# Optimization experiments

Measured on AMD Instinct MI355X. Metric: run time of the kernel, lower is better.

The kernel has to match this reference:

```python
import jax, jax.numpy as jnp
import numpy as np

B, S, D = 2, 2048, 1024
H, L = 16, 64  # num_heads, latent_dim (head dim); head_dim = H*L = 1024
ROPE_BASE = 10000.0


def _rope_tables(seq_len, dim):
    inv_freq = 1.0 / (ROPE_BASE ** (2.0 * jnp.arange(0, dim // 2, dtype=jnp.float32) / dim))
    pos = jnp.arange(seq_len, dtype=jnp.float32)
    ang = pos[:, None] * inv_freq[None, :]           # [S, L/2]
    cos = jnp.cos(ang).reshape(1, seq_len, 1, dim // 2)
    sin = jnp.sin(ang).reshape(1, seq_len, 1, dim // 2)
    return cos, sin


def _apply_rope(t, cos, sin):
    # t: [B, S, H, L]; interleaved-pair rotation then concat halves (as in source)
    tr = t.reshape(*t.shape[:-1], -1, 2)             # [B,S,H,L/2,2]
    x0, x1 = tr[..., 0], tr[..., 1]
    out = jnp.concatenate([x0 * cos - x1 * sin, x0 * sin + x1 * cos], axis=-1)
    return out.reshape(t.shape)


def setup_inputs() -> dict:
    key = jax.random.key(0)
    ks = jax.random.split(key, 5)
    scale = 0.03  # ~xavier for 1024x1024
    return {
        "x": jax.random.normal(ks[0], (B, S, D), dtype=jnp.float32),
        "Wq": jax.random.normal(ks[1], (D, H * L), dtype=jnp.float32) * scale,
        "bq": jnp.zeros((H * L,), dtype=jnp.float32),
        "Wk": jax.random.normal(ks[2], (D, H * L), dtype=jnp.float32) * scale,
        "bk": jnp.zeros((H * L,), dtype=jnp.float32),
        "Wv": jax.random.normal(ks[3], (D, H * L), dtype=jnp.float32) * scale,
        "bv": jnp.zeros((H * L,), dtype=jnp.float32),
        "Wo": jax.random.normal(ks[4], (H * L, D), dtype=jnp.float32) * scale,
        "bo": jnp.zeros((D,), dtype=jnp.float32),
    }


def reference(x, Wq, bq, Wk, bk, Wv, bv, Wo, bo):
    b, s, _ = x.shape
    q = (x @ Wq + bq).reshape(b, s, H, L)
    k = (x @ Wk + bk).reshape(b, s, H, L)
    v = (x @ Wv + bv).reshape(b, s, H, L)
    cos, sin = _rope_tables(s, L)
    q = _apply_rope(q, cos, sin)
    k = _apply_rope(k, cos, sin)
    q = jnp.transpose(q, (0, 2, 1, 3))  # [B,H,S,L]
    k = jnp.transpose(k, (0, 2, 1, 3))
    v = jnp.transpose(v, (0, 2, 1, 3))
    scores = jnp.einsum('bnqd,bnkd->bnqk', q, k) / jnp.sqrt(jnp.float32(L))
    # causal mask: keep positions where key <= query
    causal = jnp.arange(s)[None, :] <= jnp.arange(s)[:, None]  # [S,S]
    scores = jnp.where(causal, scores, -1e9)
    attn = jax.nn.softmax(scores, axis=-1)
    attended = jnp.einsum('bnqk,bnkd->bnqd', attn, v)
    attended = jnp.transpose(attended, (0, 2, 1, 3)).reshape(b, s, H * L)
    return attended @ Wo + bo
```

## Files before the change

### kernel.cpp

```cpp
#include <hip/hip_runtime.h>
#include <hip/hip_bf16.h>

typedef __bf16 bf16_t;
typedef __bf16 bf16x2 __attribute__((ext_vector_type(2)));
typedef __bf16 bf16x4 __attribute__((ext_vector_type(4)));
typedef __bf16 bf16x8 __attribute__((ext_vector_type(8)));
typedef float  f32x4  __attribute__((ext_vector_type(4)));

#define GLDS16(gp, lp) __builtin_amdgcn_global_load_lds( \
    (const __attribute__((address_space(1))) void*)(gp), \
    (__attribute__((address_space(3))) void*)(lp), 16, 0, 0)

#define MFMA16(a, b, c) __builtin_amdgcn_mfma_f32_16x16x32_bf16((a), (b), (c), 0, 0, 0)

static constexpr int kB = 2, kS = 2048, kD = 1024, kH = 16, kL = 64;
static constexpr int kM = kB * kS;
static constexpr int kNqkv = 3 * kD;
static constexpr int kBH = kB * kH;

__global__ void cast_x_kernel(const float* __restrict__ x, bf16_t* __restrict__ xb) {
    int i = blockIdx.x * 256 + threadIdx.x;
    float4 v = ((const float4*)x)[i];
    bf16x4 o;
    o[0] = (bf16_t)v.x; o[1] = (bf16_t)v.y; o[2] = (bf16_t)v.z; o[3] = (bf16_t)v.w;
    ((bf16x4*)xb)[i] = o;
}

__global__ void wtrans_kernel(const float* __restrict__ W, bf16_t* __restrict__ Wt) {
    __shared__ float t[32 * 33];
    const int k0 = blockIdx.x * 32, n0 = blockIdx.y * 32;
    const int tid = threadIdx.x;
#pragma unroll
    for (int i = 0; i < 4; ++i) {
        int idx = i * 256 + tid;
        int r = idx >> 5, c = idx & 31;
        t[r * 33 + c] = W[(size_t)(k0 + r) * 1024 + n0 + c];
    }
    __syncthreads();
#pragma unroll
    for (int i = 0; i < 4; ++i) {
        int idx = i * 256 + tid;
        int r = idx >> 5, c = idx & 31;
        Wt[(size_t)(n0 + r) * 1024 + k0 + c] = (bf16_t)t[c * 33 + r];
    }
}

__global__ void rope_table_kernel(float* __restrict__ cosT, float* __restrict__ sinT) {
    int i = blockIdx.x * 256 + threadIdx.x;
    int s = i >> 5, j = i & 31;
    double inv = pow(10000.0, -2.0 * (double)j / 64.0);
    double ang = (double)s * inv;
    cosT[i] = (float)cos(ang);
    sinT[i] = (float)sin(ang);
}

template <int MODE>
__global__ __launch_bounds__(256, 2)
void gemm_bf16(const bf16_t* __restrict__ A, const bf16_t* __restrict__ Bt,
               void* __restrict__ Cout,
               const float* __restrict__ b0, const float* __restrict__ b1,
               const float* __restrict__ b2, int Ndim, int Kdim) {
    __shared__ __align__(16) bf16_t Alds[128 * 32];
    __shared__ __align__(16) bf16_t Blds[128 * 32];
    const int tid = threadIdx.x;
    const int lane = tid & 63;
    const int wid = tid >> 6;
    const int lo = lane & 15, hi = lane >> 4;
    const int bm = blockIdx.x, bn = blockIdx.y;
    const int wr = wid >> 1, wc = wid & 1;

    const int rowS = (wid * 2) * 16 + (lane >> 2);
    const int colE = (lane & 3) * 8;
    const bf16_t* gA0 = A + (size_t)(bm * 128 + rowS) * Kdim + colE;
    const bf16_t* gA1 = gA0 + (size_t)16 * Kdim;
    const bf16_t* gB0 = Bt + (size_t)(bn * 128 + rowS) * Kdim + colE;
    const bf16_t* gB1 = gB0 + (size_t)16 * Kdim;
    bf16_t* lA0 = &Alds[(wid * 2) * 512];
    bf16_t* lA1 = &Alds[(wid * 2 + 1) * 512];
    bf16_t* lB0 = &Blds[(wid * 2) * 512];
    bf16_t* lB1 = &Blds[(wid * 2 + 1) * 512];

    f32x4 acc[4][4];
#pragma unroll
    for (int m = 0; m < 4; ++m)
#pragma unroll
        for (int n = 0; n < 4; ++n) acc[m][n] = (f32x4){0.f, 0.f, 0.f, 0.f};

    const int nk = Kdim >> 5;
    for (int kt = 0; kt < nk; ++kt) {
        const int k0 = kt * 32;
        GLDS16(gA0 + k0, lA0);
        GLDS16(gA1 + k0, lA1);
        GLDS16(gB0 + k0, lB0);
        GLDS16(gB1 + k0, lB1);
        __syncthreads();
        bf16x8 aF[4], bF[4];
#pragma unroll
        for (int m = 0; m < 4; ++m)
            aF[m] = *(const bf16x8*)&Alds[(wr * 64 + m * 16 + lo) * 32 + hi * 8];
#pragma unroll
        for (int n = 0; n < 4; ++n)
            bF[n] = *(const bf16x8*)&Blds[(wc * 64 + n * 16 + lo) * 32 + hi * 8];
#pragma unroll
        for (int m = 0; m < 4; ++m)
#pragma unroll
            for (int n = 0; n < 4; ++n)
                acc[m][n] = MFMA16(aF[m], bF[n], acc[m][n]);
        __syncthreads();
    }

    const int rbase = bm * 128 + wr * 64 + hi * 4;
    const int cbase = bn * 128 + wc * 64 + lo;
    if (MODE == 0) {
        bf16_t* C = (bf16_t*)Cout;
#pragma unroll
        for (int m = 0; m < 4; ++m)
#pragma unroll
            for (int n = 0; n < 4; ++n) {
                const int col = cbase + n * 16;
                const float bias = (col < 1024) ? b0[col]
                                 : (col < 2048) ? b1[col - 1024] : b2[col - 2048];
#pragma unroll
                for (int r = 0; r < 4; ++r) {
                    const int row = rbase + m * 16 + r;
                    C[(size_t)row * Ndim + col] = (bf16_t)(acc[m][n][r] + bias);
                }
            }
    } else {
        float* C = (float*)Cout;
#pragma unroll
        for (int m = 0; m < 4; ++m)
#pragma unroll
            for (int n = 0; n < 4; ++n) {
                const int col = cbase + n * 16;
                const float bias = b0[col];
#pragma unroll
                for (int r = 0; r < 4; ++r) {
                    const int row = rbase + m * 16 + r;
                    C[(size_t)row * Ndim + col] = acc[m][n][r] + bias;
                }
            }
    }
}

__global__ __launch_bounds__(256)
void rope_qk_kernel(const bf16_t* __restrict__ qkv,
                    const float* __restrict__ cosT,
                    const float* __restrict__ sinT,
                    bf16_t* __restrict__ Qr, bf16_t* __restrict__ Kr) {
    const int st = blockIdx.x, bh = blockIdx.y;
    const int b = bh >> 4, h = bh & 15;
    const int tid = threadIdx.x;
    const int r = tid >> 2;
    const int part = tid & 3;
    const int s = st * 64 + r;
    const int bs = b * kS + s;
    const bf16_t* qp = qkv + (size_t)bs * kNqkv + h * 64 + part * 16;
    const bf16_t* kp = qp + 1024;
    const size_t outoff = ((size_t)(b * kH + h) * kS + s) * 64;
    bf16_t* qo = Qr + outoff;
    char*   kob = (char*)(Kr + outoff);
    const float* cr = cosT + s * 32 + part * 8;
    const float* sr = sinT + s * 32 + part * 8;
    const float kScale = 0.125f * 1.44269504f;

    bf16x8 q0 = *(const bf16x8*)qp;
    bf16x8 q1 = *(const bf16x8*)(qp + 8);
    bf16x8 k0 = *(const bf16x8*)kp;
    bf16x8 k1 = *(const bf16x8*)(kp + 8);
    bf16x8 qlo, qhi, klo, khi;
#pragma unroll
    for (int j = 0; j < 8; ++j) {
        const float cv = cr[j];
        const float sv = sr[j];
        float qa, qb2, ka, kb2;
        if (j < 4) {
            qa = (float)q0[2 * j];     qb2 = (float)q0[2 * j + 1];
            ka = (float)k0[2 * j];     kb2 = (float)k0[2 * j + 1];
        } else {
            qa = (float)q1[2 * j - 8]; qb2 = (float)q1[2 * j - 7];
            ka = (float)k1[2 * j - 8]; kb2 = (float)k1[2 * j - 7];
        }
        qlo[j] = (bf16_t)((qa * cv - qb2 * sv) * kScale);
        qhi[j] = (bf16_t)((qa * sv + qb2 * cv) * kScale);
        klo[j] = (bf16_t)(ka * cv - kb2 * sv);
        khi[j] = (bf16_t)(ka * sv + kb2 * cv);
    }
    *(bf16x8*)(qo + part * 8)      = qlo;
    *(bf16x8*)(qo + 32 + part * 8) = qhi;
    const int sw = s & 7;
    *(bf16x8*)(kob + (((part)     ^ sw) << 4)) = klo;
    *(bf16x8*)(kob + (((part + 4) ^ sw) << 4)) = khi;
}

__global__ void vtrans_kernel(const bf16_t* __restrict__ qkv, bf16_t* __restrict__ VT) {
    __shared__ __align__(16) bf16_t t[64 * 72];
    const int st = blockIdx.x, bh = blockIdx.y;
    const int b = bh >> 4, h = bh & 15;
    const int tid = threadIdx.x;
    const int r = tid >> 2, g = tid & 3;
    const bf16_t* src = qkv + ((size_t)(b * kS + st * 64 + r)) * kNqkv + 2048 + h * 64 + g * 16;
    bf16x8 v0 = *(const bf16x8*)src;
    bf16x8 v1 = *(const bf16x8*)(src + 8);
    *(bf16x8*)&t[r * 72 + g * 16] = v0;
    *(bf16x8*)&t[r * 72 + g * 16 + 8] = v1;
    __syncthreads();
    bf16x8 o0, o1;
#pragma unroll
    for (int j = 0; j < 8; ++j) {
        o0[j] = t[(g * 16 + j) * 72 + r];
        o1[j] = t[(g * 16 + 8 + j) * 72 + r];
    }
    char* dstb = (char*)(VT + ((size_t)bh * 64 + r) * kS) + st * 128;
    const int sw = r & 7;
    *(bf16x8*)(dstb + (((g * 2)     ^ sw) << 4)) = o0;
    *(bf16x8*)(dstb + (((g * 2 + 1) ^ sw) << 4)) = o1;
}

__global__ __launch_bounds__(256, 2)
void attn_kernel(const bf16_t* __restrict__ Qr, const bf16_t* __restrict__ Kr,
                 const bf16_t* __restrict__ VT, bf16_t* __restrict__ attended) {
    __shared__ __align__(16) bf16_t Klds[2][64 * 64];
    __shared__ __align__(16) bf16_t Vlds[2][64 * 64];
    __shared__ __align__(16) bf16_t Plds[8][16 * 72];
    const int qp = blockIdx.x, bh = blockIdx.y;
    const int qA = qp, qB = 31 - qp;
    const int tid = threadIdx.x;
    const int lane = tid & 63, wid = tid >> 6;
    const int lo = lane & 15, hi = lane >> 4;
    const int q0A = qA * 64 + wid * 16;
    const int q0B = qB * 64 + wid * 16;

    const char* Kg = (const char*)(Kr + (size_t)bh * kS * 64);
    const char* Vg = (const char*)(VT + (size_t)bh * 64 * kS);
    const bf16_t* Q = Qr + (size_t)bh * kS * 64;

    const bf16x8 aQA0 = *(const bf16x8*)&Q[(size_t)(q0A + lo) * 64 + hi * 8];
    const bf16x8 aQA1 = *(const bf16x8*)&Q[(size_t)(q0A + lo) * 64 + 32 + hi * 8];
    const bf16x8 aQB0 = *(const bf16x8*)&Q[(size_t)(q0B + lo) * 64 + hi * 8];
    const bf16x8 aQB1 = *(const bf16x8*)&Q[(size_t)(q0B + lo) * 64 + 32 + hi * 8];

    f32x4 OA[4], OB[4];
#pragma unroll
    for (int dt = 0; dt < 4; ++dt) {
        OA[dt] = (f32x4){0.f, 0.f, 0.f, 0.f};
        OB[dt] = (f32x4){0.f, 0.f, 0.f, 0.f};
    }
    float mA = -1e30f, lA = 0.f, mB = -1e30f, lB = 0.f;

    auto stage = [&](int buf, int t) {
        char* Kl = (char*)&Klds[buf][0];
        char* Vl = (char*)&Vlds[buf][0];
        const size_t kb = (size_t)t * 128 * 64;
        const int vcol = t * 128;
#pragma unroll
        for (int j = 0; j < 2; ++j) {
            const int seg = wid * 2 + j;
            GLDS16(Kg + kb + seg * 1024 + lane * 16, Kl + seg * 1024);
            const int row = seg * 8 + (lane >> 3);
            GLDS16(Vg + (size_t)row * (kS * 2) + vcol + (lane & 7) * 16, Vl + seg * 1024);
        }
    };

    auto softmax = [&](f32x4 (&s)[4], float& m_run, float& l_run, f32x4 (&O)[4],
                       int q0, bool edge, int kv0, bf16_t* Pl,
                       bf16x8& aP0, bf16x8& aP1) {
        if (edge) {
            const int qg = q0 + lo;
#pragma unroll
            for (int ct = 0; ct < 4; ++ct)
#pragma unroll
                for (int r = 0; r < 4; ++r)
                    if (kv0 + ct * 16 + hi * 4 + r > qg) s[ct][r] = -1e30f;
        }
        float pmax = -1e30f;
#pragma unroll
        for (int ct = 0; ct < 4; ++ct)
#pragma unroll
            for (int r = 0; r < 4; ++r) pmax = fmaxf(pmax, s[ct][r]);
        pmax = fmaxf(pmax, __shfl_xor(pmax, 16, 64));
        pmax = fmaxf(pmax, __shfl_xor(pmax, 32, 64));
        if (!__all(pmax - m_run <= 8.0f)) {
            const float mn = fmaxf(m_run, pmax);
            const float alpha = exp2f(m_run - mn);
            m_run = mn;
            l_run *= alpha;
            float av[4];
#pragma unroll
            for (int r = 0; r < 4; ++r) av[r] = __shfl(alpha, hi * 4 + r, 64);
#pragma unroll
            for (int dt = 0; dt < 4; ++dt)
#pragma unroll
                for (int r = 0; r < 4; ++r) O[dt][r] *= av[r];
        }
        float psum = 0.f;
#pragma unroll
        for (int ct = 0; ct < 4; ++ct)
#pragma unroll
            for (int r = 0; r < 4; ++r) {
                const float e = exp2f(s[ct][r] - m_run);
                s[ct][r] = e;
                psum += e;
            }
        psum += __shfl_xor(psum, 16, 64);
        psum += __shfl_xor(psum, 32, 64);
        l_run += psum;
#pragma unroll
        for (int ct = 0; ct < 4; ++ct)
#pragma unroll
            for (int rp = 0; rp < 2; ++rp) {
                bf16x2 v;
                v[0] = (bf16_t)s[ct][2 * rp];
                v[1] = (bf16_t)s[ct][2 * rp + 1];
                *(bf16x2*)&Pl[lo * 72 + ct * 16 + hi * 4 + 2 * rp] = v;
            }
        aP0 = *(const bf16x8*)&Pl[lo * 72 + hi * 8];
        aP1 = *(const bf16x8*)&Pl[lo * 72 + 32 + hi * 8];
    };

    stage(0, 0);
    int cur = 0;
    for (int t = 0; t <= qB; ++t) {
        __syncthreads();
        if (t < qB) stage(cur ^ 1, t + 1);
        const char* Kb = (const char*)&Klds[cur][0];
        const char* Vb = (const char*)&Vlds[cur][0];
        const bool actA = (t <= qA);
        const int kv0 = t * 64;

        f32x4 sB[4], sA[4];
#pragma unroll
        for (int ct = 0; ct < 4; ++ct) {
            sB[ct] = (f32x4){0.f, 0.f, 0.f, 0.f};
            sA[ct] = (f32x4){0.f, 0.f, 0.f, 0.f};
        }
#pragma unroll
        for (int ct = 0; ct < 4; ++ct) {
            const int rr = ct * 16 + lo;
            const bf16x8 bK0 = *(const bf16x8*)(Kb + rr * 128 + (((hi)     ^ (rr & 7)) << 4));
            const bf16x8 bK1 = *(const bf16x8*)(Kb + rr * 128 + (((hi + 4) ^ (rr & 7)) << 4));
            sB[ct] = MFMA16(bK0, aQB0, sB[ct]);
            sB[ct] = MFMA16(bK1, aQB1, sB[ct]);
            if (actA) {
                sA[ct] = MFMA16(bK0, aQA0, sA[ct]);
                sA[ct] = MFMA16(bK1, aQA1, sA[ct]);
            }
        }

        bf16x8 aP0A, aP1A, aP0B, aP1B;
        if (actA) softmax(sA, mA, lA, OA, q0A, t == qA, kv0, &Plds[wid * 2][0], aP0A, aP1A);
        softmax(sB, mB, lB, OB, q0B, t == qB, kv0, &Plds[wid * 2 + 1][0], aP0B, aP1B);

#pragma unroll
        for (int dt = 0; dt < 4; ++dt) {
            const int rr = dt * 16 + lo;
            const bf16x8 bV0 = *(const bf16x8*)(Vb + rr * 128 + (((hi)     ^ (rr & 7)) << 4));
            const bf16x8 bV1 = *(const bf16x8*)(Vb + rr * 128 + (((hi + 4) ^ (rr & 7)) << 4));
            OB[dt] = MFMA16(aP0B, bV0, OB[dt]);
            OB[dt] = MFMA16(aP1B, bV1, OB[dt]);
            if (actA) {
                OA[dt] = MFMA16(aP0A, bV0, OA[dt]);
                OA[dt] = MFMA16(aP1A, bV1, OA[dt]);
            }
        }
        cur ^= 1;
    }

    const int b = bh >> 4, h = bh & 15;
    float liA[4], liB[4];
#pragma unroll
    for (int r = 0; r < 4; ++r) {
        liA[r] = 1.0f / __shfl(lA, hi * 4 + r, 64);
        liB[r] = 1.0f / __shfl(lB, hi * 4 + r, 64);
    }
#pragma unroll
    for (int dt = 0; dt < 4; ++dt)
#pragma unroll
        for (int r = 0; r < 4; ++r) {
            const int rowA = q0A + hi * 4 + r;
            const int rowB = q0B + hi * 4 + r;
            attended[((size_t)(b * kS + rowA)) * kD + h * 64 + dt * 16 + lo] =
                (bf16_t)(OA[dt][r] * liA[r]);
            attended[((size_t)(b * kS + rowB)) * kD + h * 64 + dt * 16 + lo] =
                (bf16_t)(OB[dt][r] * liB[r]);
        }
}

extern "C" void kernel_launch(void* const* d_in, const int* in_sizes, int n_in,
                              void* d_out, int out_size, void* d_ws, size_t ws_size,
                              hipStream_t stream) {
    const float* x  = (const float*)d_in[0];
    const float* Wq = (const float*)d_in[1];
    const float* bq = (const float*)d_in[2];
    const float* Wk = (const float*)d_in[3];
    const float* bk = (const float*)d_in[4];
    const float* Wv = (const float*)d_in[5];
    const float* bv = (const float*)d_in[6];
    const float* Wo = (const float*)d_in[7];
    const float* bo = (const float*)d_in[8];
    float* out = (float*)d_out;

    char* ws = (char*)d_ws;
    size_t off = 0;
    auto carve = [&](size_t bytes) -> char* {
        char* p = ws + off;
        off += (bytes + 255) & ~(size_t)255;
        return p;
    };
    bf16_t* xb    = (bf16_t*)carve((size_t)kM * kD * 2);
    bf16_t* WqkvT = (bf16_t*)carve((size_t)kNqkv * kD * 2);
    bf16_t* WoT   = (bf16_t*)carve((size_t)kD * kD * 2);
    float*  cosT  = (float*)carve((size_t)kS * 32 * 4);
    float*  sinT  = (float*)carve((size_t)kS * 32 * 4);
    bf16_t* qkv   = (bf16_t*)carve((size_t)kM * kNqkv * 2);
    bf16_t* Qr    = (bf16_t*)carve((size_t)kBH * kS * 64 * 2);
    bf16_t* Kr    = (bf16_t*)carve((size_t)kBH * kS * 64 * 2);
    bf16_t* VT    = (bf16_t*)carve((size_t)kBH * kS * 64 * 2);
    bf16_t* att   = (bf16_t*)carve((size_t)kM * kD * 2);

    cast_x_kernel<<<(kM * kD) / (256 * 4), 256, 0, stream>>>(x, xb);
    wtrans_kernel<<<dim3(32, 32), 256, 0, stream>>>(Wq, WqkvT);
    wtrans_kernel<<<dim3(32, 32), 256, 0, stream>>>(Wk, WqkvT + (size_t)1024 * 1024);
    wtrans_kernel<<<dim3(32, 32), 256, 0, stream>>>(Wv, WqkvT + (size_t)2048 * 1024);
    wtrans_kernel<<<dim3(32, 32), 256, 0, stream>>>(Wo, WoT);
    rope_table_kernel<<<(kS * 32) / 256, 256, 0, stream>>>(cosT, sinT);

    gemm_bf16<0><<<dim3(kM / 128, kNqkv / 128), 256, 0, stream>>>(
        xb, WqkvT, qkv, bq, bk, bv, kNqkv, kD);

    rope_qk_kernel<<<dim3(kS / 64, kBH), 256, 0, stream>>>(qkv, cosT, sinT, Qr, Kr);
    vtrans_kernel<<<dim3(kS / 64, kBH), 256, 0, stream>>>(qkv, VT);

    attn_kernel<<<dim3(16, kBH), 256, 0, stream>>>(Qr, Kr, VT, att);

    gemm_bf16<1><<<dim3(kM / 128, kD / 128), 256, 0, stream>>>(
        att, WoT, out, bo, nullptr, nullptr, kD, kD);
}
```

Measured before the change: 147.1 us.

## Load K and V fragments directly from global memory instead of LDS staging

Removes the double-buffered LDS staging of K and V tiles in the attention kernel. Each wave now loads its MFMA operand fragments straight from global memory into registers, and the XOR swizzle is dropped from the rope and V-transpose writers to match. It also raises wave priority around the MFMA sections with s_setprio. This drops block-wide barriers and LDS traffic, but each wave of the block now fetches the same K/V data, so it depends on L1/L2 hits and exposes global load latency without a prefetch.

```diff
diff --git a/kernel.cpp b/kernel.cpp
--- a/kernel.cpp
+++ b/kernel.cpp
@@ -159,7 +159,7 @@
     const bf16_t* kp = qp + 1024;
     const size_t outoff = ((size_t)(b * kH + h) * kS + s) * 64;
     bf16_t* qo = Qr + outoff;
-    char*   kob = (char*)(Kr + outoff);
+    bf16_t* ko = Kr + outoff;
     const float* cr = cosT + s * 32 + part * 8;
     const float* sr = sinT + s * 32 + part * 8;
     const float kScale = 0.125f * 1.44269504f;
@@ -188,9 +188,8 @@
     }
     *(bf16x8*)(qo + part * 8)      = qlo;
     *(bf16x8*)(qo + 32 + part * 8) = qhi;
-    const int sw = s & 7;
-    *(bf16x8*)(kob + (((part)     ^ sw) << 4)) = klo;
-    *(bf16x8*)(kob + (((part + 4) ^ sw) << 4)) = khi;
+    *(bf16x8*)(ko + part * 8)      = klo;
+    *(bf16x8*)(ko + 32 + part * 8) = khi;
 }
 
 __global__ void vtrans_kernel(const bf16_t* __restrict__ qkv, bf16_t* __restrict__ VT) {
@@ -211,17 +210,14 @@
         o0[j] = t[(g * 16 + j) * 72 + r];
         o1[j] = t[(g * 16 + 8 + j) * 72 + r];
     }
-    char* dstb = (char*)(VT + ((size_t)bh * 64 + r) * kS) + st * 128;
-    const int sw = r & 7;
-    *(bf16x8*)(dstb + (((g * 2)     ^ sw) << 4)) = o0;
-    *(bf16x8*)(dstb + (((g * 2 + 1) ^ sw) << 4)) = o1;
+    bf16_t* dst = VT + ((size_t)bh * 64 + r) * kS + st * 64 + g * 16;
+    *(bf16x8*)dst = o0;
+    *(bf16x8*)(dst + 8) = o1;
 }
 
 __global__ __launch_bounds__(256, 2)
 void attn_kernel(const bf16_t* __restrict__ Qr, const bf16_t* __restrict__ Kr,
                  const bf16_t* __restrict__ VT, bf16_t* __restrict__ attended) {
-    __shared__ __align__(16) bf16_t Klds[2][64 * 64];
-    __shared__ __align__(16) bf16_t Vlds[2][64 * 64];
     __shared__ __align__(16) bf16_t Plds[8][16 * 72];
     const int qp = blockIdx.x, bh = blockIdx.y;
     const int qA = qp, qB = 31 - qp;
@@ -231,9 +227,9 @@
     const int q0A = qA * 64 + wid * 16;
     const int q0B = qB * 64 + wid * 16;
 
-    const char* Kg = (const char*)(Kr + (size_t)bh * kS * 64);
-    const char* Vg = (const char*)(VT + (size_t)bh * 64 * kS);
-    const bf16_t* Q = Qr + (size_t)bh * kS * 64;
+    const bf16_t* Kp = Kr + (size_t)bh * kS * 64;
+    const bf16_t* Vp = VT + (size_t)bh * 64 * kS;
+    const bf16_t* Q  = Qr + (size_t)bh * kS * 64;
 
     const bf16x8 aQA0 = *(const bf16x8*)&Q[(size_t)(q0A + lo) * 64 + hi * 8];
     const bf16x8 aQA1 = *(const bf16x8*)&Q[(size_t)(q0A + lo) * 64 + 32 + hi * 8];
@@ -247,20 +243,6 @@
         OB[dt] = (f32x4){0.f, 0.f, 0.f, 0.f};
     }
     float mA = -1e30f, lA = 0.f, mB = -1e30f, lB = 0.f;
-
-    auto stage = [&](int buf, int t) {
-        char* Kl = (char*)&Klds[buf][0];
-        char* Vl = (char*)&Vlds[buf][0];
-        const size_t kb = (size_t)t * 128 * 64;
-        const int vcol = t * 128;
-#pragma unroll
-        for (int j = 0; j < 2; ++j) {
-            const int seg = wid * 2 + j;
-            GLDS16(Kg + kb + seg * 1024 + lane * 16, Kl + seg * 1024);
-            const int row = seg * 8 + (lane >> 3);
-            GLDS16(Vg + (size_t)row * (kS * 2) + vcol + (lane & 7) * 16, Vl + seg * 1024);
-        }
-    };
 
     auto softmax = [&](f32x4 (&s)[4], float& m_run, float& l_run, f32x4 (&O)[4],
                        int q0, bool edge, int kv0, bf16_t* Pl,
@@ -318,15 +300,17 @@
         aP1 = *(const bf16x8*)&Pl[lo * 72 + 32 + hi * 8];
     };
 
-    stage(0, 0);
-    int cur = 0;
     for (int t = 0; t <= qB; ++t) {
-        __syncthreads();
-        if (t < qB) stage(cur ^ 1, t + 1);
-        const char* Kb = (const char*)&Klds[cur][0];
-        const char* Vb = (const char*)&Vlds[cur][0];
+        const int kv0 = t * 64;
         const bool actA = (t <= qA);
-        const int kv0 = t * 64;
+
+        bf16x8 bK0[4], bK1[4];
+#pragma unroll
+        for (int ct = 0; ct < 4; ++ct) {
+            const bf16_t* kr = Kp + (size_t)(kv0 + ct * 16 + lo) * 64 + hi * 8;
+            bK0[ct] = *(const bf16x8*)kr;
+            bK1[ct] = *(const bf16x8*)(kr + 32);
+        }
 
         f32x4 sB[4], sA[4];
 #pragma unroll
@@ -334,36 +318,41 @@
             sB[ct] = (f32x4){0.f, 0.f, 0.f, 0.f};
             sA[ct] = (f32x4){0.f, 0.f, 0.f, 0.f};
         }
+        __builtin_amdgcn_s_setprio(1);
 #pragma unroll
         for (int ct = 0; ct < 4; ++ct) {
-            const int rr = ct * 16 + lo;
-            const bf16x8 bK0 = *(const bf16x8*)(Kb + rr * 128 + (((hi)     ^ (rr & 7)) << 4));
-            const bf16x8 bK1 = *(const bf16x8*)(Kb + rr * 128 + (((hi + 4) ^ (rr & 7)) << 4));
-            sB[ct] = MFMA16(bK0, aQB0, sB[ct]);
-            sB[ct] = MFMA16(bK1, aQB1, sB[ct]);
+            sB[ct] = MFMA16(bK0[ct], aQB0, sB[ct]);
+            sB[ct] = MFMA16(bK1[ct], aQB1, sB[ct]);
             if (actA) {
-                sA[ct] = MFMA16(bK0, aQA0, sA[ct]);
-                sA[ct] = MFMA16(bK1, aQA1, sA[ct]);
-            }
+                sA[ct] = MFMA16(bK0[ct], aQA0, sA[ct]);
+                sA[ct] = MFMA16(bK1[ct], aQA1, sA[ct]);
+            }
+        }
+        __builtin_amdgcn_s_setprio(0);
+
+        bf16x8 bV0[4], bV1[4];
+#pragma unroll
+        for (int dt = 0; dt < 4; ++dt) {
+            const bf16_t* vr = Vp + (size_t)(dt * 16 + lo) * kS + kv0 + hi * 8;
+            bV0[dt] = *(const bf16x8*)vr;
+            bV1[dt] = *(const bf16x8*)(vr + 32);
         }
 
         bf16x8 aP0A, aP1A, aP0B, aP1B;
         if (actA) softmax(sA, mA, lA, OA, q0A, t == qA, kv0, &Plds[wid * 2][0], aP0A, aP1A);
         softmax(sB, mB, lB, OB, q0B, t == qB, kv0, &Plds[wid * 2 + 1][0], aP0B, aP1B);
 
+        __builtin_amdgcn_s_setprio(1);
 #pragma unroll
         for (int dt = 0; dt < 4; ++dt) {
-            const int rr = dt * 16 + lo;
-            const bf16x8 bV0 = *(const bf16x8*)(Vb + rr * 128 + (((hi)     ^ (rr & 7)) << 4));
-            const bf16x8 bV1 = *(const bf16x8*)(Vb + rr * 128 + (((hi + 4) ^ (rr & 7)) << 4));
-            OB[dt] = MFMA16(aP0B, bV0, OB[dt]);
-            OB[dt] = MFMA16(aP1B, bV1, OB[dt]);
+            OB[dt] = MFMA16(aP0B, bV0[dt], OB[dt]);
+            OB[dt] = MFMA16(aP1B, bV1[dt], OB[dt]);
             if (actA) {
-                OA[dt] = MFMA16(aP0A, bV0, OA[dt]);
-                OA[dt] = MFMA16(aP1A, bV1, OA[dt]);
-            }
-        }
-        cur ^= 1;
+                OA[dt] = MFMA16(aP0A, bV0[dt], OA[dt]);
+                OA[dt] = MFMA16(aP1A, bV1[dt], OA[dt]);
+            }
+        }
+        __builtin_amdgcn_s_setprio(0);
     }
 
     const int b = bh >> 4, h = bh & 15;
```

Measured after the change: 205.8 us. 1.4x slower.

## Replace paired-tile attention blocks with one query tile per block, heavy-first order

Applied to the files above, without the earlier changes.

The attention kernel stops pairing query tiles qp and 31-qp in each block and gives each block a single 64-row query tile. The grid becomes (32 heads*batch, 32 tiles), with the longest causal tiles dispatched first, and launch bounds are raised to allow 4 blocks per CU. MFMA sections are wrapped in s_setprio hints, and the P scratch buffer loses its padding. This doubles the block count and cuts per-block registers to improve occupancy and load balance. In exchange, K/V tiles are no longer shared between two query tiles, so global and LDS traffic increases, and the unpadded P layout may cause bank conflicts.

```diff
diff --git a/kernel.cpp b/kernel.cpp
--- a/kernel.cpp
+++ b/kernel.cpp
@@ -217,36 +217,32 @@
     *(bf16x8*)(dstb + (((g * 2 + 1) ^ sw) << 4)) = o1;
 }
 
-__global__ __launch_bounds__(256, 2)
+__global__ __launch_bounds__(256, 4)
 void attn_kernel(const bf16_t* __restrict__ Qr, const bf16_t* __restrict__ Kr,
                  const bf16_t* __restrict__ VT, bf16_t* __restrict__ attended) {
     __shared__ __align__(16) bf16_t Klds[2][64 * 64];
     __shared__ __align__(16) bf16_t Vlds[2][64 * 64];
-    __shared__ __align__(16) bf16_t Plds[8][16 * 72];
-    const int qp = blockIdx.x, bh = blockIdx.y;
-    const int qA = qp, qB = 31 - qp;
+    __shared__ __align__(16) bf16_t Plds[4][16 * 64];
+    const int bh = blockIdx.x;
+    const int qt = 31 - blockIdx.y;
     const int tid = threadIdx.x;
     const int lane = tid & 63, wid = tid >> 6;
     const int lo = lane & 15, hi = lane >> 4;
-    const int q0A = qA * 64 + wid * 16;
-    const int q0B = qB * 64 + wid * 16;
+    const int q0 = qt * 64 + wid * 16;
 
     const char* Kg = (const char*)(Kr + (size_t)bh * kS * 64);
     const char* Vg = (const char*)(VT + (size_t)bh * 64 * kS);
     const bf16_t* Q = Qr + (size_t)bh * kS * 64;
 
-    const bf16x8 aQA0 = *(const bf16x8*)&Q[(size_t)(q0A + lo) * 64 + hi * 8];
-    const bf16x8 aQA1 = *(const bf16x8*)&Q[(size_t)(q0A + lo) * 64 + 32 + hi * 8];
-    const bf16x8 aQB0 = *(const bf16x8*)&Q[(size_t)(q0B + lo) * 64 + hi * 8];
-    const bf16x8 aQB1 = *(const bf16x8*)&Q[(size_t)(q0B + lo) * 64 + 32 + hi * 8];
-
-    f32x4 OA[4], OB[4];
-#pragma unroll
-    for (int dt = 0; dt < 4; ++dt) {
-        OA[dt] = (f32x4){0.f, 0.f, 0.f, 0.f};
-        OB[dt] = (f32x4){0.f, 0.f, 0.f, 0.f};
-    }
-    float mA = -1e30f, lA = 0.f, mB = -1e30f, lB = 0.f;
+    const bf16x8 aQ0 = *(const bf16x8*)&Q[(size_t)(q0 + lo) * 64 + hi * 8];
+    const bf16x8 aQ1 = *(const bf16x8*)&Q[(size_t)(q0 + lo) * 64 + 32 + hi * 8];
+
+    bf16_t* Pl = &Plds[wid][0];
+
+    f32x4 O[4];
+#pragma unroll
+    for (int dt = 0; dt < 4; ++dt) O[dt] = (f32x4){0.f, 0.f, 0.f, 0.f};
+    float m_run = -1e30f, l_run = 0.f;
 
     auto stage = [&](int buf, int t) {
         char* Kl = (char*)&Klds[buf][0];
@@ -262,9 +258,31 @@
         }
     };
 
-    auto softmax = [&](f32x4 (&s)[4], float& m_run, float& l_run, f32x4 (&O)[4],
-                       int q0, bool edge, int kv0, bf16_t* Pl,
-                       bf16x8& aP0, bf16x8& aP1) {
+    stage(0, 0);
+    int cur = 0;
+    const int ntiles = qt + 1;
+    for (int t = 0; t < ntiles; ++t) {
+        __syncthreads();
+        if (t + 1 < ntiles) stage(cur ^ 1, t + 1);
+        const char* Kb = (const char*)&Klds[cur][0];
+        const char* Vb = (const char*)&Vlds[cur][0];
+        const int kv0 = t * 64;
+        const bool edge = (t == qt);
+
+        f32x4 s[4];
+#pragma unroll
+        for (int ct = 0; ct < 4; ++ct) s[ct] = (f32x4){0.f, 0.f, 0.f, 0.f};
+        __builtin_amdgcn_s_setprio(1);
+#pragma unroll
+        for (int ct = 0; ct < 4; ++ct) {
+            const int rr = ct * 16 + lo;
+            const bf16x8 bK0 = *(const bf16x8*)(Kb + rr * 128 + (((hi)     ^ (rr & 7)) << 4));
+            const bf16x8 bK1 = *(const bf16x8*)(Kb + rr * 128 + (((hi + 4) ^ (rr & 7)) << 4));
+            s[ct] = MFMA16(bK0, aQ0, s[ct]);
+            s[ct] = MFMA16(bK1, aQ1, s[ct]);
+        }
+        __builtin_amdgcn_s_setprio(0);
+
         if (edge) {
             const int qg = q0 + lo;
 #pragma unroll
@@ -312,77 +330,35 @@
                 bf16x2 v;
                 v[0] = (bf16_t)s[ct][2 * rp];
                 v[1] = (bf16_t)s[ct][2 * rp + 1];
-                *(bf16x2*)&Pl[lo * 72 + ct * 16 + hi * 4 + 2 * rp] = v;
+                *(bf16x2*)&Pl[lo * 64 + ct * 16 + hi * 4 + 2 * rp] = v;
             }
-        aP0 = *(const bf16x8*)&Pl[lo * 72 + hi * 8];
-        aP1 = *(const bf16x8*)&Pl[lo * 72 + 32 + hi * 8];
-    };
-
-    stage(0, 0);
-    int cur = 0;
-    for (int t = 0; t <= qB; ++t) {
-        __syncthreads();
-        if (t < qB) stage(cur ^ 1, t + 1);
-        const char* Kb = (const char*)&Klds[cur][0];
-        const char* Vb = (const char*)&Vlds[cur][0];
-        const bool actA = (t <= qA);
-        const int kv0 = t * 64;
-
-        f32x4 sB[4], sA[4];
-#pragma unroll
-        for (int ct = 0; ct < 4; ++ct) {
-            sB[ct] = (f32x4){0.f, 0.f, 0.f, 0.f};
-            sA[ct] = (f32x4){0.f, 0.f, 0.f, 0.f};
-        }
-#pragma unroll
-        for (int ct = 0; ct < 4; ++ct) {
-            const int rr = ct * 16 + lo;
-            const bf16x8 bK0 = *(const bf16x8*)(Kb + rr * 128 + (((hi)     ^ (rr & 7)) << 4));
-            const bf16x8 bK1 = *(const bf16x8*)(Kb + rr * 128 + (((hi + 4) ^ (rr & 7)) << 4));
-            sB[ct] = MFMA16(bK0, aQB0, sB[ct]);
-            sB[ct] = MFMA16(bK1, aQB1, sB[ct]);
-            if (actA) {
-                sA[ct] = MFMA16(bK0, aQA0, sA[ct]);
-                sA[ct] = MFMA16(bK1, aQA1, sA[ct]);
-            }
-        }
-
-        bf16x8 aP0A, aP1A, aP0B, aP1B;
-        if (actA) softmax(sA, mA, lA, OA, q0A, t == qA, kv0, &Plds[wid * 2][0], aP0A, aP1A);
-        softmax(sB, mB, lB, OB, q0B, t == qB, kv0, &Plds[wid * 2 + 1][0], aP0B, aP1B);
-
+        const bf16x8 aP0 = *(const bf16x8*)&Pl[lo * 64 + hi * 8];
+        const bf16x8 aP1 = *(const bf16x8*)&Pl[lo * 64 + 32 + hi * 8];
+
+        __builtin_amdgcn_s_setprio(1);
 #pragma unroll
         for (int dt = 0; dt < 4; ++dt) {
             const int rr = dt * 16 + lo;
             const bf16x8 bV0 = *(const bf16x8*)(Vb + rr * 128 + (((hi)     ^ (rr & 7)) << 4));
             const bf16x8 bV1 = *(const bf16x8*)(Vb + rr * 128 + (((hi + 4) ^ (rr & 7)) << 4));
-            OB[dt] = MFMA16(aP0B, bV0, OB[dt]);
-            OB[dt] = MFMA16(aP1B, bV1, OB[dt]);
-            if (actA) {
-                OA[dt] = MFMA16(aP0A, bV0, OA[dt]);
-                OA[dt] = MFMA16(aP1A, bV1, OA[dt]);
-            }
-        }
+            O[dt] = MFMA16(aP0, bV0, O[dt]);
+            O[dt] = MFMA16(aP1, bV1, O[dt]);
+        }
+        __builtin_amdgcn_s_setprio(0);
         cur ^= 1;
     }
 
     const int b = bh >> 4, h = bh & 15;
-    float liA[4], liB[4];
-#pragma unroll
-    for (int r = 0; r < 4; ++r) {
-        liA[r] = 1.0f / __shfl(lA, hi * 4 + r, 64);
-        liB[r] = 1.0f / __shfl(lB, hi * 4 + r, 64);
-    }
+    float li[4];
+#pragma unroll
+    for (int r = 0; r < 4; ++r) li[r] = 1.0f / __shfl(l_run, hi * 4 + r, 64);
 #pragma unroll
     for (int dt = 0; dt < 4; ++dt)
 #pragma unroll
         for (int r = 0; r < 4; ++r) {
-            const int rowA = q0A + hi * 4 + r;
-            const int rowB = q0B + hi * 4 + r;
-            attended[((size_t)(b * kS + rowA)) * kD + h * 64 + dt * 16 + lo] =
-                (bf16_t)(OA[dt][r] * liA[r]);
-            attended[((size_t)(b * kS + rowB)) * kD + h * 64 + dt * 16 + lo] =
-                (bf16_t)(OB[dt][r] * liB[r]);
+            const int row = q0 + hi * 4 + r;
+            attended[((size_t)(b * kS + row)) * kD + h * 64 + dt * 16 + lo] =
+                (bf16_t)(O[dt][r] * li[r]);
         }
 }
 
@@ -431,7 +407,7 @@
     rope_qk_kernel<<<dim3(kS / 64, kBH), 256, 0, stream>>>(qkv, cosT, sinT, Qr, Kr);
     vtrans_kernel<<<dim3(kS / 64, kBH), 256, 0, stream>>>(qkv, VT);
 
-    attn_kernel<<<dim3(16, kBH), 256, 0, stream>>>(Qr, Kr, VT, att);
+    attn_kernel<<<dim3(kBH, 32), 256, 0, stream>>>(Qr, Kr, VT, att);
 
     gemm_bf16<1><<<dim3(kM / 128, kD / 128), 256, 0, stream>>>(
         att, WoT, out, bo, nullptr, nullptr, kD, kD);
```

New measurement: 165.3 us. 1.12x slower.
